# Performance work log

Hardware: AMD Instinct MI355X
Metric: run time of the kernel (lower is better)

The kernel has to match this reference:

```python
import jax, jax.numpy as jnp
import numpy as np

B, N1, N2, D = 8, 2048, 2048, 512

def setup_inputs() -> dict:
    key = jax.random.key(0)
    k1, k2, k3, k4 = jax.random.split(key, 4)
    input1 = jax.random.normal(k1, (B, N1, D), dtype=jnp.float32)
    input2 = jax.random.normal(k2, (B, N2, D), dtype=jnp.float32)
    # nn.Linear(D, D): weight [D, D] (out, in), bias [D]
    W_w = jax.random.normal(k3, (D, D), dtype=jnp.float32) * (1.0 / np.sqrt(D))
    W_b = jax.random.normal(k4, (D,), dtype=jnp.float32) * 0.01
    return {"input1": input1, "input2": input2, "W_w": W_w, "W_b": W_b}

def reference(input1, input2, W_w, W_b):
    # q = W(input1): [B, N1, D]
    q = jnp.einsum('bnd,od->bno', input1, W_w) + W_b
    # unscaled scores softmax over last dim (keys N2)
    attn = jax.nn.softmax(jnp.einsum('bnd,bmd->bnm', q, input2), axis=-1)  # [B, N1, N2]
    output1 = jnp.einsum('bnm,bmd->bnd', attn, input2)   # [B, N1, D]
    output2 = jnp.einsum('bnm,bnd->bmd', attn, input1)   # attn^T @ input1 -> [B, N2, D]
    return (output1, output2)
```

## Files before the change

### kernel.cpp

```cpp
#include <hip/hip_runtime.h>


typedef _Float16 f16x8 __attribute__((ext_vector_type(8)));
typedef _Float16 f16x4 __attribute__((ext_vector_type(4)));
typedef float floatx4 __attribute__((ext_vector_type(4)));
typedef __attribute__((address_space(1))) const void* gptr_t;
typedef __attribute__((address_space(3))) void* lptr_t;

union F8 { f16x8 v; _Float16 h[8]; unsigned short u[8]; unsigned w[4]; };
union F4 { f16x4 v; _Float16 h[4]; unsigned u2[2]; };

__device__ __forceinline__ void gld16(const void* g, void* l) {
    __builtin_amdgcn_global_load_lds((gptr_t)g, (lptr_t)l, 16, 0, 0);
}
__device__ __forceinline__ floatx4 mfma16(f16x8 a, f16x8 b, floatx4 c) {
    return __builtin_amdgcn_mfma_f32_16x16x32_f16(a, b, c, 0, 0, 0);
}

template <int ROWS>
__device__ __forceinline__ void stage64(const _Float16* g, int ldg,
                                        _Float16* lds, int tid) {
#pragma unroll
    for (int c = 0; c < (ROWS * 8) / 256; ++c) {
        const int q = c * 256 + tid;
        const int row = q >> 3;
        const int oct = (q & 7) ^ (row & 7);
        gld16(g + (size_t)row * ldg + oct * 8, lds + q * 8);
    }
}
__device__ __forceinline__ f16x8 ldfrag64(const _Float16* lds, int row, int j) {
    return *(const f16x8*)&lds[row * 64 + ((j ^ (row & 7)) << 3)];
}
__device__ __forceinline__ f16x8 ldfragA(const _Float16* lds, int row, int j) {
    return *(const f16x8*)&lds[row * 64 + ((j ^ ((row >> 1) & 7)) << 3)];
}

#define TS 66
__global__ __launch_bounds__(256) void k_prep2(
    const float* __restrict__ in1, const float* __restrict__ in2,
    _Float16* __restrict__ x16, _Float16* __restrict__ xt,
    _Float16* __restrict__ k16, _Float16* __restrict__ vt,
    const float* __restrict__ Ww, _Float16* __restrict__ w16)
{
    __shared__ __align__(16) _Float16 T[64 * TS];
    const int z = blockIdx.z;
    const int t = threadIdx.x;
    if (z == 16) {
        const int flat = blockIdx.y * 8 + blockIdx.x;
        if (flat < 128) {
            const size_t i = ((size_t)flat * 256 + t) * 8;
            float4 a = *(const float4*)(Ww + i);
            float4 b = *(const float4*)(Ww + i + 4);
            F8 w;
            w.h[0] = (_Float16)a.x; w.h[1] = (_Float16)a.y;
            w.h[2] = (_Float16)a.z; w.h[3] = (_Float16)a.w;
            w.h[4] = (_Float16)b.x; w.h[5] = (_Float16)b.y;
            w.h[6] = (_Float16)b.z; w.h[7] = (_Float16)b.w;
            *(f16x8*)(w16 + i) = w.v;
        }
        return;
    }
    const int b = z & 7;
    const float* src = (z < 8 ? in1 : in2);
    _Float16* rowo = (z < 8 ? x16 : k16);
    _Float16* colo = (z < 8 ? xt : vt);
    const int d0 = blockIdx.x * 64, n0 = blockIdx.y * 64;
    const float* Sp = src + (size_t)b * 2048 * 512;
    _Float16* Rp = rowo + (size_t)b * 2048 * 512;
    _Float16* Cp = colo + (size_t)b * 512 * 2048;

#pragma unroll
    for (int c = 0; c < 4; c++) {
        const int q = c * 256 + t, r = q >> 4, c4 = q & 15;
        const float4 g = *(const float4*)(Sp + (size_t)(n0 + r) * 512 + d0 + c4 * 4);
        F4 w;
        w.h[0] = (_Float16)g.x; w.h[1] = (_Float16)g.y;
        w.h[2] = (_Float16)g.z; w.h[3] = (_Float16)g.w;
        *(f16x4*)(Rp + (size_t)(n0 + r) * 512 + d0 + c4 * 4) = w.v;
        *(unsigned*)&T[r * TS + c4 * 4]     = w.u2[0];
        *(unsigned*)&T[r * TS + c4 * 4 + 2] = w.u2[1];
    }
    __syncthreads();
    const int c8 = t & 7, drp = (t >> 3) * 2;
    F8 w0, w1;
#pragma unroll
    for (int i = 0; i < 8; i++) {
        const unsigned g = *(const unsigned*)&T[(c8 * 8 + i) * TS + drp];
        w0.u[i] = (unsigned short)(g & 0xffffu);
        w1.u[i] = (unsigned short)(g >> 16);
    }
    *(f16x8*)(Cp + (size_t)(d0 + drp) * 2048 + n0 + c8 * 8) = w0.v;
    *(f16x8*)(Cp + (size_t)(d0 + drp + 1) * 2048 + n0 + c8 * 8) = w1.v;
}

__global__ __launch_bounds__(256, 4) void k_qgemm16(
    const _Float16* __restrict__ A, const _Float16* __restrict__ W,
    const float* __restrict__ bias, _Float16* __restrict__ q)
{
    __shared__ __align__(16) _Float16 As[128 * 64], Bs[128 * 64];
    const int tid = threadIdx.x;
    const int lane = tid & 63, wave = tid >> 6;
    const int wM = (wave >> 1) * 64, wN = (wave & 1) * 64;
    const int lrow = lane & 15, kq = lane >> 4;
    const int bi = blockIdx.x;
    const int r0 = (bi >> 2) * 128, c0 = (bi & 3) * 128;

    floatx4 acc[4][4];
#pragma unroll
    for (int i = 0; i < 4; i++)
#pragma unroll
        for (int j = 0; j < 4; j++) acc[i][j] = (floatx4){0.f, 0.f, 0.f, 0.f};

    for (int k0 = 0; k0 < 512; k0 += 64) {
        stage64<128>(A + (size_t)r0 * 512 + k0, 512, As, tid);
        stage64<128>(W + (size_t)c0 * 512 + k0, 512, Bs, tid);
        __syncthreads();
#pragma unroll
        for (int ks = 0; ks < 2; ks++) {
            f16x8 a[4], b[4];
#pragma unroll
            for (int i = 0; i < 4; i++) {
                a[i] = ldfrag64(As, wM + i * 16 + lrow, ks * 4 + kq);
                b[i] = ldfrag64(Bs, wN + i * 16 + lrow, ks * 4 + kq);
            }
#pragma unroll
            for (int mi = 0; mi < 4; mi++)
#pragma unroll
                for (int ni = 0; ni < 4; ni++)
                    acc[mi][ni] = mfma16(a[mi], b[ni], acc[mi][ni]);
        }
        __syncthreads();
    }
#pragma unroll
    for (int ni = 0; ni < 4; ni++) {
        const int col = c0 + wN + ni * 16 + lrow;
        const float bv = bias[col];
#pragma unroll
        for (int mi = 0; mi < 4; mi++) {
            const int row = r0 + wM + mi * 16 + kq * 4;
#pragma unroll
            for (int r = 0; r < 4; r++)
                q[(size_t)(row + r) * 512 + col] = (_Float16)(acc[mi][ni][r] + bv);
        }
    }
}

__global__ __launch_bounds__(256, 2) void k_scores16(
    const _Float16* __restrict__ q, const _Float16* __restrict__ k,
    _Float16* __restrict__ S)
{
    __shared__ __align__(16) _Float16 lds[24576];
    const int tid = threadIdx.x;
    const int lane = tid & 63, wave = tid >> 6;
    const int wM = (wave >> 1) * 64, wN = (wave & 1) * 128;
    const int lrow = lane & 15, kq = lane >> 4;
    const int bi = blockIdx.x;
    const int bz = bi & 7, t = bi >> 3;
    const int c0 = (t & 7) * 256, r0 = (t >> 3) * 128;
    const _Float16* qp = q + (size_t)bz * 2048 * 512;
    const _Float16* kp = k + (size_t)bz * 2048 * 512;
    _Float16* Sp = S + (size_t)bz * 2048 * 2048;

    floatx4 acc[4][8];
#pragma unroll
    for (int i = 0; i < 4; i++)
#pragma unroll
        for (int j = 0; j < 8; j++) acc[i][j] = (floatx4){0.f, 0.f, 0.f, 0.f};

    for (int k0 = 0; k0 < 512; k0 += 64) {
        stage64<128>(qp + (size_t)r0 * 512 + k0, 512, lds, tid);
        stage64<256>(kp + (size_t)c0 * 512 + k0, 512, lds + 8192, tid);
        __syncthreads();
#pragma unroll
        for (int ks = 0; ks < 2; ks++) {
            f16x8 a[4], b[8];
#pragma unroll
            for (int i = 0; i < 4; i++)
                a[i] = ldfrag64(lds, wM + i * 16 + lrow, ks * 4 + kq);
#pragma unroll
            for (int i = 0; i < 8; i++)
                b[i] = ldfrag64(lds + 8192, wN + i * 16 + lrow, ks * 4 + kq);
#pragma unroll
            for (int mi = 0; mi < 4; mi++)
#pragma unroll
                for (int ni = 0; ni < 8; ni++)
                    acc[mi][ni] = mfma16(a[mi], b[ni], acc[mi][ni]);
        }
        __syncthreads();
    }
#pragma unroll
    for (int mi = 0; mi < 4; mi++)
#pragma unroll
        for (int ni = 0; ni < 8; ni++) {
            const int row = r0 + wM + mi * 16 + kq * 4;
            const int col = c0 + wN + ni * 16 + lrow;
            _Float16* dst = Sp + (size_t)row * 2048 + col;
#pragma unroll
            for (int r = 0; r < 4; r++) dst[(size_t)r * 2048] = (_Float16)acc[mi][ni][r];
        }
}

__global__ __launch_bounds__(256) void k_softmax(const _Float16* __restrict__ S,
                                                 _Float16* __restrict__ P)
{
    const int wave = threadIdx.x >> 6, lane = threadIdx.x & 63;
    const int row = blockIdx.x * 4 + wave;
    const _Float16* s = S + (size_t)row * 2048;
    _Float16* p = P + (size_t)row * 2048;

    F8 raw[4];
    float v[32];
#pragma unroll
    for (int c = 0; c < 4; c++) {
        raw[c].v = *(const f16x8*)(s + c * 512 + lane * 8);
#pragma unroll
        for (int i = 0; i < 8; i++) v[c * 8 + i] = (float)raw[c].h[i];
    }
    float m = v[0];
#pragma unroll
    for (int i = 1; i < 32; i++) m = fmaxf(m, v[i]);
#pragma unroll
    for (int off = 32; off >= 1; off >>= 1) m = fmaxf(m, __shfl_xor(m, off));

    float sum = 0.f;
#pragma unroll
    for (int i = 0; i < 32; i++) { v[i] = __expf(v[i] - m); sum += v[i]; }
#pragma unroll
    for (int off = 32; off >= 1; off >>= 1) sum += __shfl_xor(sum, off);
    const float inv = 1.0f / sum;

#pragma unroll
    for (int c = 0; c < 4; c++) {
        F8 w;
#pragma unroll
        for (int i = 0; i < 8; i++) w.h[i] = (_Float16)(v[c * 8 + i] * inv);
        *(f16x8*)(p + c * 512 + lane * 8) = w.v;
    }
}

__device__ __forceinline__ void loadtr16(const _Float16* Pp, int r0, int mPair,
                                         int kBase, int k0, unsigned (&u)[16]) {
#pragma unroll
    for (int j = 0; j < 16; j++)
        u[j] = *(const unsigned*)(
            Pp + (size_t)(k0 + kBase + j) * 2048 + r0 + mPair);
}

__global__ __launch_bounds__(256, 2) void k_out12(
    const _Float16* __restrict__ P, const _Float16* __restrict__ Vt,
    const _Float16* __restrict__ Xt, float* __restrict__ O1,
    float* __restrict__ O2)
{
    __shared__ __align__(16) _Float16 lds[24576];
    const int tid = threadIdx.x;
    const int lane = tid & 63, wave = tid >> 6;
    const int wM = (wave >> 1) * 64, wN = (wave & 1) * 128;
    const int lrow = lane & 15, kq = lane >> 4;
    const bool isO2 = blockIdx.x & 1;
    const int bi = blockIdx.x >> 1;
    const int bz = bi & 7, t = bi >> 3;
    const int c0 = (t & 1) * 256, r0 = (t >> 1) * 128;
    const _Float16* Pp = P + (size_t)bz * 2048 * 2048;
    const _Float16* Bp = (isO2 ? Xt : Vt) + (size_t)bz * 512 * 2048;
    float* Op = (isO2 ? O2 : O1) + (size_t)bz * 2048 * 512;

    floatx4 acc[4][8];
#pragma unroll
    for (int i = 0; i < 4; i++)
#pragma unroll
        for (int j = 0; j < 8; j++) acc[i][j] = (floatx4){0.f, 0.f, 0.f, 0.f};

    if (!isO2) {
        for (int k0 = 0; k0 < 2048; k0 += 64) {
            stage64<128>(Pp + (size_t)r0 * 2048 + k0, 2048, lds, tid);
            stage64<256>(Bp + (size_t)c0 * 2048 + k0, 2048, lds + 8192, tid);
            __syncthreads();
#pragma unroll
            for (int ks = 0; ks < 2; ks++) {
                f16x8 a[4], b[8];
#pragma unroll
                for (int i = 0; i < 4; i++)
                    a[i] = ldfrag64(lds, wM + i * 16 + lrow, ks * 4 + kq);
#pragma unroll
                for (int i = 0; i < 8; i++)
                    b[i] = ldfrag64(lds + 8192, wN + i * 16 + lrow, ks * 4 + kq);
#pragma unroll
                for (int mi = 0; mi < 4; mi++)
#pragma unroll
                    for (int ni = 0; ni < 8; ni++)
                        acc[mi][ni] = mfma16(a[mi], b[ni], acc[mi][ni]);
            }
            __syncthreads();
        }
    } else {
        _Float16* As_ = lds;
        const int mPair = (tid & 63) * 2;
        const int kBase = (tid >> 6) * 16;

        unsigned u[16];
        loadtr16(Pp, r0, mPair, kBase, 0, u);
        for (int k0 = 0; k0 < 2048; k0 += 64) {
            const int sw = (mPair >> 1) & 7;
#pragma unroll
            for (int half = 0; half < 2; half++) {
                const int oct = (kBase >> 3) + half;
                F8 w0, w1;
#pragma unroll
                for (int j = 0; j < 8; j++) {
                    const unsigned g = u[half * 8 + j];
                    w0.u[j] = (unsigned short)(g & 0xffffu);
                    w1.u[j] = (unsigned short)(g >> 16);
                }
                *(f16x8*)&As_[mPair * 64 + ((oct ^ sw) << 3)] = w0.v;
                *(f16x8*)&As_[(mPair + 1) * 64 + ((oct ^ sw) << 3)] = w1.v;
            }
            stage64<256>(Bp + (size_t)c0 * 2048 + k0, 2048, lds + 8192, tid);
            __syncthreads();
            if (k0 < 2048 - 64)
                loadtr16(Pp, r0, mPair, kBase, k0 + 64, u);
#pragma unroll
            for (int ks = 0; ks < 2; ks++) {
                f16x8 a[4], b[8];
#pragma unroll
                for (int i = 0; i < 4; i++)
                    a[i] = ldfragA(As_, wM + i * 16 + lrow, ks * 4 + kq);
#pragma unroll
                for (int i = 0; i < 8; i++)
                    b[i] = ldfrag64(lds + 8192, wN + i * 16 + lrow, ks * 4 + kq);
#pragma unroll
                for (int mi = 0; mi < 4; mi++)
#pragma unroll
                    for (int ni = 0; ni < 8; ni++)
                        acc[mi][ni] = mfma16(a[mi], b[ni], acc[mi][ni]);
            }
            __syncthreads();
        }
    }
#pragma unroll
    for (int mi = 0; mi < 4; mi++)
#pragma unroll
        for (int ni = 0; ni < 8; ni++) {
            const int row = r0 + wM + mi * 16 + kq * 4;
            const int col = c0 + wN + ni * 16 + lrow;
            float* dst = Op + (size_t)row * 512 + col;
#pragma unroll
            for (int r = 0; r < 4; r++) dst[(size_t)r * 512] = acc[mi][ni][r];
        }
}

extern "C" void kernel_launch(void* const* d_in, const int* in_sizes, int n_in,
                              void* d_out, int out_size, void* d_ws, size_t ws_size,
                              hipStream_t stream)
{
    (void)in_sizes; (void)n_in; (void)out_size; (void)ws_size;
    const float* in1 = (const float*)d_in[0];
    const float* in2 = (const float*)d_in[1];
    const float* Ww  = (const float*)d_in[2];
    const float* Wb  = (const float*)d_in[3];
    float* out = (float*)d_out;

    char* ws = (char*)d_ws;
    _Float16* S   = (_Float16*)ws;
    _Float16* P   = (_Float16*)(ws + 67108864ull);
    _Float16* q16 = (_Float16*)(ws + 134217728ull);
    _Float16* x16 = (_Float16*)(ws + 150994944ull);
    _Float16* k16 = (_Float16*)(ws + 167772160ull);
    _Float16* vt  = (_Float16*)(ws + 184549376ull);
    _Float16* xt  = (_Float16*)(ws + 201326592ull);
    _Float16* w16 = (_Float16*)(ws + 218103808ull);

    k_prep2<<<dim3(8, 32, 17), 256, 0, stream>>>(in1, in2, x16, xt, k16, vt, Ww, w16);
    k_qgemm16<<<512, 256, 0, stream>>>(x16, w16, Wb, q16);
    k_scores16<<<1024, 256, 0, stream>>>(q16, k16, S);
    k_softmax<<<4096, 256, 0, stream>>>(S, P);
    k_out12<<<512, 256, 0, stream>>>(P, vt, xt, out, out + 8388608);
}
```

Measured before the change: 256.4 us.

## Rewrite scores GEMM as 8-wave 256x256 tile with multi-stage prefetch pipeline

Replaces the 128x256 single-buffered scores kernel with a 512-thread, 256x256 output tile kernel that double-buffers the K dimension in 32-wide half stages. Loads for upcoming stages are issued while MFMAs run, gated by explicit vmcnt waits and raw s_barrier calls, and MFMA phases get raised wave priority. This aims to hide global-load latency and increase operand reuse per LDS byte, at the cost of 128KB LDS per block and fragile manual synchronisation.

```diff
diff --git a/kernel.cpp b/kernel.cpp
--- a/kernel.cpp
+++ b/kernel.cpp
@@ -33,6 +33,20 @@
 }
 __device__ __forceinline__ f16x8 ldfragA(const _Float16* lds, int row, int j) {
     return *(const f16x8*)&lds[row * 64 + ((j ^ ((row >> 1) & 7)) << 3)];
+}
+
+__device__ __forceinline__ void stage_half(const _Float16* g, int ldg,
+                                           _Float16* lds, int tid) {
+#pragma unroll
+    for (int c = 0; c < 2; ++c) {
+        const int u = c * 512 + tid;
+        const int row = u >> 2;
+        const int oct = (u & 3) ^ ((row >> 1) & 3);
+        gld16(g + (size_t)row * ldg + oct * 8, lds + u * 8);
+    }
+}
+__device__ __forceinline__ f16x8 ldfrag32(const _Float16* lds, int row, int kq) {
+    return *(const f16x8*)&lds[row * 32 + ((kq ^ ((row >> 1) & 3)) << 3)];
 }
 
 #define TS 66
@@ -145,55 +159,84 @@
     }
 }
 
-__global__ __launch_bounds__(256, 2) void k_scores16(
+__global__ __launch_bounds__(512, 2) void k_scores8p(
     const _Float16* __restrict__ q, const _Float16* __restrict__ k,
     _Float16* __restrict__ S)
 {
-    __shared__ __align__(16) _Float16 lds[24576];
+    __shared__ __align__(16) _Float16 lds[65536];
     const int tid = threadIdx.x;
     const int lane = tid & 63, wave = tid >> 6;
-    const int wM = (wave >> 1) * 64, wN = (wave & 1) * 128;
+    const int wr = wave >> 2, wc = wave & 3;
     const int lrow = lane & 15, kq = lane >> 4;
     const int bi = blockIdx.x;
-    const int bz = bi & 7, t = bi >> 3;
-    const int c0 = (t & 7) * 256, r0 = (t >> 3) * 128;
-    const _Float16* qp = q + (size_t)bz * 2048 * 512;
-    const _Float16* kp = k + (size_t)bz * 2048 * 512;
+    const int bz = bi & 7, t0 = bi >> 3;
+    const int c0 = (t0 & 7) * 256, r0 = (t0 >> 3) * 256;
+    const _Float16* qp = q + (size_t)bz * 2048 * 512 + (size_t)r0 * 512;
+    const _Float16* kp = k + (size_t)bz * 2048 * 512 + (size_t)c0 * 512;
     _Float16* Sp = S + (size_t)bz * 2048 * 2048;
 
-    floatx4 acc[4][8];
-#pragma unroll
-    for (int i = 0; i < 4; i++)
-#pragma unroll
-        for (int j = 0; j < 8; j++) acc[i][j] = (floatx4){0.f, 0.f, 0.f, 0.f};
-
-    for (int k0 = 0; k0 < 512; k0 += 64) {
-        stage64<128>(qp + (size_t)r0 * 512 + k0, 512, lds, tid);
-        stage64<256>(kp + (size_t)c0 * 512 + k0, 512, lds + 8192, tid);
-        __syncthreads();
-#pragma unroll
-        for (int ks = 0; ks < 2; ks++) {
-            f16x8 a[4], b[8];
-#pragma unroll
-            for (int i = 0; i < 4; i++)
-                a[i] = ldfrag64(lds, wM + i * 16 + lrow, ks * 4 + kq);
-#pragma unroll
-            for (int i = 0; i < 8; i++)
-                b[i] = ldfrag64(lds + 8192, wN + i * 16 + lrow, ks * 4 + kq);
-#pragma unroll
-            for (int mi = 0; mi < 4; mi++)
-#pragma unroll
-                for (int ni = 0; ni < 8; ni++)
-                    acc[mi][ni] = mfma16(a[mi], b[ni], acc[mi][ni]);
-        }
-        __syncthreads();
-    }
-#pragma unroll
-    for (int mi = 0; mi < 4; mi++)
-#pragma unroll
-        for (int ni = 0; ni < 8; ni++) {
-            const int row = r0 + wM + mi * 16 + kq * 4;
-            const int col = c0 + wN + ni * 16 + lrow;
+    floatx4 acc[8][4];
+#pragma unroll
+    for (int i = 0; i < 8; i++)
+#pragma unroll
+        for (int j = 0; j < 4; j++) acc[i][j] = (floatx4){0.f, 0.f, 0.f, 0.f};
+
+#define STAGE_H(h)                                                             \
+    do {                                                                       \
+        const int th_ = (h) >> 2, s_ = (h) & 3, kh_ = s_ >> 1;                 \
+        const _Float16* src_ = (s_ & 1) ? kp : qp;                             \
+        _Float16* dst_ = lds + ((s_ & 1) ? 32768 : 0) + (th_ & 1) * 16384 +    \
+                         kh_ * 8192;                                           \
+        stage_half(src_ + th_ * 64 + kh_ * 32, 512, dst_, tid);                \
+    } while (0)
+
+#pragma unroll
+    for (int h = 0; h < 6; ++h) STAGE_H(h);
+
+    for (int t = 0; t < 8; ++t) {
+        const int p = t & 1;
+#pragma unroll
+        for (int kh = 0; kh < 2; ++kh) {
+            f16x8 bfr[4];
+#pragma unroll
+            for (int mh = 0; mh < 2; ++mh) {
+                const int h = t * 4 + kh * 2 + mh + 6;
+                if (h < 32) STAGE_H(h);
+                if (kh == 0 && mh == 0) {
+                    if (t == 7) asm volatile("s_waitcnt vmcnt(0)" ::: "memory");
+                    else        asm volatile("s_waitcnt vmcnt(6)" ::: "memory");
+                }
+                __builtin_amdgcn_s_barrier();
+                const _Float16* Ab = lds + p * 16384 + kh * 8192;
+                const _Float16* Bb = lds + 32768 + p * 16384 + kh * 8192;
+                if (mh == 0) {
+#pragma unroll
+                    for (int ni = 0; ni < 4; ni++)
+                        bfr[ni] = ldfrag32(Bb, wc * 64 + ni * 16 + lrow, kq);
+                }
+                f16x8 afr[4];
+#pragma unroll
+                for (int mi = 0; mi < 4; mi++)
+                    afr[mi] = ldfrag32(Ab, wr * 128 + mh * 64 + mi * 16 + lrow, kq);
+                __builtin_amdgcn_s_setprio(1);
+#pragma unroll
+                for (int mi = 0; mi < 4; mi++)
+#pragma unroll
+                    for (int ni = 0; ni < 4; ni++)
+                        acc[mh * 4 + mi][ni] =
+                            mfma16(afr[mi], bfr[ni], acc[mh * 4 + mi][ni]);
+                __builtin_amdgcn_s_setprio(0);
+                __builtin_amdgcn_s_barrier();
+            }
+        }
+    }
+#undef STAGE_H
+#pragma unroll
+    for (int mi = 0; mi < 8; mi++)
+#pragma unroll
+        for (int ni = 0; ni < 4; ni++) {
+            const int row = r0 + wr * 128 + mi * 16 + kq * 4;
+            const int col = c0 + wc * 64 + ni * 16 + lrow;
             _Float16* dst = Sp + (size_t)row * 2048 + col;
 #pragma unroll
             for (int r = 0; r < 4; r++) dst[(size_t)r * 2048] = (_Float16)acc[mi][ni][r];
@@ -371,7 +414,7 @@
 
     k_prep2<<<dim3(8, 32, 17), 256, 0, stream>>>(in1, in2, x16, xt, k16, vt, Ww, w16);
     k_qgemm16<<<512, 256, 0, stream>>>(x16, w16, Wb, q16);
-    k_scores16<<<1024, 256, 0, stream>>>(q16, k16, S);
+    k_scores8p<<<512, 512, 0, stream>>>(q16, k16, S);
     k_softmax<<<4096, 256, 0, stream>>>(S, P);
     k_out12<<<512, 256, 0, stream>>>(P, vt, xt, out, out + 8388608);
 }
```

After: 267.4 us. +4.3%, slower.
